# Performance work log

Measured on AMD Instinct MI355X. Metric: run time of the kernel, lower is better.

The kernel has to match this reference:

```python
import jax, jax.numpy as jnp
import numpy as np

IN_SIZE = 784
Z_DIM = 128
K_DIM = 8192
BATCH = 16384
ENC_HIDDEN = [512, 256]          # EncoderMLP default
DEC_SIZES = [Z_DIM, 256, 512, 784]  # DecoderMLP default: [latent, *hidden]


def _linear(x, w, b):
    return x @ w + b


def find_nearest(query, target):
    # Faithful to: sqrt(sum((Q-T)^2, -1)).min(1)[1]; sqrt is monotone so
    # argmin of squared distance is identical. Computed via the GEMM
    # expansion instead of materializing the (N,K,D) broadcast tensor.
    q2 = jnp.sum(query * query, axis=1, keepdims=True)        # [N,1]
    t2 = jnp.sum(target * target, axis=1)                     # [K]
    d2 = q2 - 2.0 * (query @ target.T) + t2[None, :]          # [N,K]
    idx = jnp.argmin(d2, axis=1)
    return target[idx]


def setup_inputs() -> dict:
    key = jax.random.key(0)
    ks = jax.random.split(key, 16)
    s = 0.02
    inp = {"X": jax.random.uniform(ks[0], (BATCH, 1, 28, 28), dtype=jnp.float32)}
    # Encoder: 784 -> 512 -> 256 (mlp blocks, ReLU) -> 128 (plain Linear)
    enc_sizes = [IN_SIZE] + ENC_HIDDEN + [Z_DIM]
    for i, (din, dout) in enumerate(zip(enc_sizes, enc_sizes[1:]), 1):
        inp[f"enc_w{i}"] = s * jax.random.normal(ks[i], (din, dout), dtype=jnp.float32)
        inp[f"enc_b{i}"] = jnp.zeros((dout,), dtype=jnp.float32)
    # Codebook
    inp["codebook"] = jax.random.normal(ks[8], (K_DIM, Z_DIM), dtype=jnp.float32)
    # Decoder: 128 -> 256 -> 512 -> 784 (mlp blocks, ReLU) + sigmoid out
    for i, (din, dout) in enumerate(zip(DEC_SIZES, DEC_SIZES[1:]), 1):
        inp[f"dec_w{i}"] = s * jax.random.normal(ks[8 + i], (din, dout), dtype=jnp.float32)
        inp[f"dec_b{i}"] = jnp.zeros((dout,), dtype=jnp.float32)
    return inp


def reference(X, enc_w1, enc_b1, enc_w2, enc_b2, enc_w3, enc_b3, codebook,
              dec_w1, dec_b1, dec_w2, dec_b2, dec_w3, dec_b3):
    x = X.reshape(-1, IN_SIZE)
    # Encoder (mlp_block = Linear+ReLU, final layer plain Linear)
    h = jax.nn.relu(_linear(x, enc_w1, enc_b1))
    h = jax.nn.relu(_linear(h, enc_w2, enc_b2))
    z_enc = _linear(h, enc_w3, enc_b3)                         # [N, Z]
    # Nearest codebook vector for each encoding
    z_dec = find_nearest(z_enc, codebook)                      # [N, Z]
    # Decoder
    d = jax.nn.relu(_linear(z_dec, dec_w1, dec_b1))
    d = jax.nn.relu(_linear(d, dec_w2, dec_b2))
    d = jax.nn.relu(_linear(d, dec_w3, dec_b3))
    x_recon = jax.nn.sigmoid(d).reshape(-1, 1, 28, 28)
    # Nearest encoding for each codebook vector (for embedding loss)
    z_enc_for_embd = find_nearest(codebook, z_enc)             # [K, Z]
    return (x_recon, z_enc, z_dec, z_enc_for_embd)
```

## Files before the change

### kernel.cpp

```cpp
#include <hip/hip_runtime.h>
#include <math.h>

using u16 = unsigned short;
using u32 = unsigned int;
using u64 = unsigned long long;

typedef __bf16 bf16x8 __attribute__((ext_vector_type(8)));
typedef short  s16x8  __attribute__((ext_vector_type(8)));
typedef float  f32x4  __attribute__((ext_vector_type(4)));

__device__ __forceinline__ float b2f(u16 u){
  union { u32 i; float f; } x; x.i = ((u32)u) << 16; return x.f;
}
__device__ __forceinline__ u16 f2b(float f){
  union { float f; u32 i; } x; x.f = f;
  u32 i = x.i;
  u32 r = (i + 0x7fffu + ((i >> 16) & 1u)) >> 16;
  return (u16)r;
}
__device__ __forceinline__ f32x4 mfma16(s16x8 a, s16x8 b, f32x4 c){
  return __builtin_amdgcn_mfma_f32_16x16x32_bf16(
      __builtin_bit_cast(bf16x8, a), __builtin_bit_cast(bf16x8, b), c, 0, 0, 0);
}
__device__ __forceinline__ u64 shfl_xor_u64(u64 v, int m){
  int lo = __shfl_xor((int)(u32)v, m);
  int hi = __shfl_xor((int)(u32)(v >> 32), m);
  return ((u64)(u32)hi << 32) | (u32)lo;
}
__device__ __forceinline__ u64 umin64(u64 a, u64 b){ return a < b ? a : b; }
__device__ __forceinline__ u64 packmin(float v, int idx){
  u32 b = __float_as_uint(v);
  b = (b & 0x80000000u) ? ~b : (b | 0x80000000u);
  return ((u64)b << 32) | (u32)idx;
}

__global__ __launch_bounds__(256) void canary_k(float* out, float code){
  out[threadIdx.x] = code;
}

__global__ __launch_bounds__(256) void prep_weights(
    const float* __restrict__ w1, const float* __restrict__ w2, const float* __restrict__ w3,
    const float* __restrict__ dw1, const float* __restrict__ dw2, const float* __restrict__ dw3,
    const float* __restrict__ cb,
    u16* __restrict__ o1h, u16* __restrict__ o1l, u16* __restrict__ o2h, u16* __restrict__ o2l,
    u16* __restrict__ o3h, u16* __restrict__ o3l, u16* __restrict__ o4h, u16* __restrict__ o4l,
    u16* __restrict__ o5h, u16* __restrict__ o5l, u16* __restrict__ o6h, u16* __restrict__ o6l,
    u16* __restrict__ cbh, u16* __restrict__ cbl)
{
  size_t o = (size_t)blockIdx.x * 256 + threadIdx.x;
  if (o >= 1155072){
    size_t e = o - 1155072;
    if (e >= 1048576) return;
    float v = cb[e];
    u16 h = f2b(v);
    cbh[e] = h;
    cbl[e] = f2b(v - b2f(h));
    return;
  }
  const float* src; u16 *hi, *lo; int K, N, Kp; size_t base;
  if      (o <  425984){ src=w1;  hi=o1h; lo=o1l; K=784; N=512; Kp=832; base=0; }
  else if (o <  557056){ src=w2;  hi=o2h; lo=o2l; K=512; N=256; Kp=512; base=425984; }
  else if (o <  589824){ src=w3;  hi=o3h; lo=o3l; K=256; N=128; Kp=256; base=557056; }
  else if (o <  622592){ src=dw1; hi=o4h; lo=o4l; K=128; N=256; Kp=128; base=589824; }
  else if (o <  753664){ src=dw2; hi=o5h; lo=o5l; K=256; N=512; Kp=256; base=622592; }
  else                 { src=dw3; hi=o6h; lo=o6l; K=512; N=784; Kp=512; base=753664; }
  size_t e = o - base;
  int n = (int)(e / Kp), kp = (int)(e % Kp);
  u16 h = 0, l = 0;
  if (kp < K){
    float v = src[(size_t)kp * N + n];
    h = f2b(v);
    l = f2b(v - b2f(h));
  }
  hi[e] = h; lo[e] = l;
}

__global__ __launch_bounds__(256) void norms_all(const float* __restrict__ z, const float* __restrict__ cb,
                                                 float* __restrict__ q2, float* __restrict__ t2){
  int i = blockIdx.x * 256 + threadIdx.x;
  const float* src; float* dst;
  if (i < 16384){ src = z + (size_t)i * 128; dst = q2 + i; }
  else { int j = i - 16384; src = cb + (size_t)j * 128; dst = t2 + j; }
  const float4* r = (const float4*)src;
  float s = 0.f;
  for (int k = 0; k < 32; k++){
    float4 p = r[k];
    s += p.x * p.x + p.y * p.y + p.z * p.z + p.w * p.w;
  }
  *dst = s;
}

template<int ACT, int OUTP>
__global__ __launch_bounds__(256, 2) void gemm_af32(
    const float* __restrict__ A, const u16* __restrict__ B0, const u16* __restrict__ B1,
    const float* __restrict__ bias, float* __restrict__ Cf,
    u16* __restrict__ P0, u16* __restrict__ P1,
    int Astr, int KLIM, int Kp, int KT, int N, int nRowsB)
{
  __shared__ __align__(16) u16 Ah[128][72];
  __shared__ __align__(16) u16 Al[128][72];
  __shared__ __align__(16) u16 Bh[128][72];
  __shared__ __align__(16) u16 Bl[128][72];
  const int tid = threadIdx.x;
  const int m0 = blockIdx.y * 128, n0 = blockIdx.x * 128;
  const int wave = tid >> 6, lane = tid & 63;
  const int wm = (wave >> 1) * 64, wn = (wave & 1) * 64;
  const int quad = lane >> 4, l15 = lane & 15;
  f32x4 acc[4][4] = {};

  for (int kt = 0; kt < KT; ++kt){
    const int kb = kt * 64;
    #pragma unroll
    for (int c = 0; c < 8; c++){
      int idx = c * 256 + tid;
      int r = idx >> 4, c4 = (idx & 15) * 4;
      float4 v = make_float4(0.f, 0.f, 0.f, 0.f);
      if (kb + c4 < KLIM)
        v = *(const float4*)(A + (size_t)(m0 + r) * Astr + kb + c4);
      ushort4 h, l;
      h.x = f2b(v.x); l.x = f2b(v.x - b2f(h.x));
      h.y = f2b(v.y); l.y = f2b(v.y - b2f(h.y));
      h.z = f2b(v.z); l.z = f2b(v.z - b2f(h.z));
      h.w = f2b(v.w); l.w = f2b(v.w - b2f(h.w));
      *(ushort4*)&Ah[r][c4] = h;
      *(ushort4*)&Al[r][c4] = l;
    }
    #pragma unroll
    for (int c = 0; c < 4; c++){
      int idx = c * 256 + tid;
      int r = idx >> 3, col = (idx & 7) * 8;
      int rb = n0 + r; rb = rb < nRowsB ? rb : nRowsB - 1;
      *(uint4*)&Bh[r][col] = *(const uint4*)(B0 + (size_t)rb * Kp + kb + col);
      *(uint4*)&Bl[r][col] = *(const uint4*)(B1 + (size_t)rb * Kp + kb + col);
    }
    __syncthreads();
    #pragma unroll
    for (int kh = 0; kh < 2; ++kh){
      s16x8 ah[4], al[4], bh[4], bl[4];
      #pragma unroll
      for (int t4 = 0; t4 < 4; t4++){
        ah[t4] = *(const s16x8*)&Ah[wm + t4 * 16 + l15][kh * 32 + quad * 8];
        al[t4] = *(const s16x8*)&Al[wm + t4 * 16 + l15][kh * 32 + quad * 8];
        bh[t4] = *(const s16x8*)&Bh[wn + t4 * 16 + l15][kh * 32 + quad * 8];
        bl[t4] = *(const s16x8*)&Bl[wn + t4 * 16 + l15][kh * 32 + quad * 8];
      }
      #pragma unroll
      for (int mt = 0; mt < 4; mt++)
        #pragma unroll
        for (int nt = 0; nt < 4; nt++){
          acc[mt][nt] = mfma16(ah[mt], bh[nt], acc[mt][nt]);
          acc[mt][nt] = mfma16(ah[mt], bl[nt], acc[mt][nt]);
          acc[mt][nt] = mfma16(al[mt], bh[nt], acc[mt][nt]);
        }
    }
    __syncthreads();
  }

  float bvs[4]; int cols[4];
  #pragma unroll
  for (int nt = 0; nt < 4; nt++){
    int cN = n0 + wn + nt * 16 + l15;
    cols[nt] = cN;
    int cc = cN < N ? cN : N - 1;
    bvs[nt] = bias[cc];
  }
  #pragma unroll
  for (int mt = 0; mt < 4; mt++){
    int rbase = m0 + wm + mt * 16 + quad * 4;
    #pragma unroll
    for (int nt = 0; nt < 4; nt++){
      if (cols[nt] < N){
        #pragma unroll
        for (int r = 0; r < 4; r++){
          float v = acc[mt][nt][r] + bvs[nt];
          if (ACT >= 1) v = v > 0.f ? v : 0.f;
          if (ACT == 2) v = 1.f / (1.f + expf(-v));
          size_t off = (size_t)(rbase + r) * N + cols[nt];
          if (OUTP == 2){
            P0[off] = f2b(v);
          } else {
            Cf[off] = v;
            if (OUTP == 1){
              u16 h = f2b(v);
              P0[off] = h;
              P1[off] = f2b(v - b2f(h));
            }
          }
        }
      }
    }
  }
}

__global__ __launch_bounds__(256, 1) void dist3(
    const u16* __restrict__ Zh, const u16* __restrict__ Zl,
    const u16* __restrict__ Bh, const u16* __restrict__ Bl,
    const float* __restrict__ q2, const float* __restrict__ t2,
    u64* __restrict__ rowp, u64* __restrict__ colp)
{
  __shared__ u64 sRow[2][128];
  const int tid = threadIdx.x;
  const int i0 = blockIdx.y * 128;
  const int strip = blockIdx.x;
  const int wave = tid >> 6, lane = tid & 63;
  const int wm = (wave >> 1) * 64, wn = (wave & 1) * 64;
  const int quad = lane >> 4, l15 = lane & 15;

  s16x8 zh[2][2][4], zl[2][2][4];
  #pragma unroll
  for (int kb = 0; kb < 2; kb++)
    #pragma unroll
    for (int kh = 0; kh < 2; kh++)
      #pragma unroll
      for (int mt = 0; mt < 4; mt++){
        size_t off = (size_t)(i0 + wm + mt * 16 + l15) * 128 + kb * 64 + kh * 32 + quad * 8;
        zh[kb][kh][mt] = *(const s16x8*)(Zh + off);
        zl[kb][kh][mt] = *(const s16x8*)(Zl + off);
      }
  float qv[4][4];
  #pragma unroll
  for (int mt = 0; mt < 4; mt++)
    #pragma unroll
    for (int r = 0; r < 4; r++)
      qv[mt][r] = q2[i0 + wm + mt * 16 + quad * 4 + r];

  u64 rowm[4][4];
  #pragma unroll
  for (int mt = 0; mt < 4; mt++)
    #pragma unroll
    for (int r = 0; r < 4; r++) rowm[mt][r] = ~0ULL;

  for (int jt = 0; jt < 16; ++jt){
    const int j0 = strip * 2048 + jt * 128;
    f32x4 acc[4][4] = {};
    #pragma unroll
    for (int kb = 0; kb < 2; kb++)
      #pragma unroll
      for (int kh = 0; kh < 2; kh++){
        s16x8 bh[4], bl[4];
        #pragma unroll
        for (int nt = 0; nt < 4; nt++){
          size_t off = (size_t)(j0 + wn + nt * 16 + l15) * 128 + kb * 64 + kh * 32 + quad * 8;
          bh[nt] = *(const s16x8*)(Bh + off);
          bl[nt] = *(const s16x8*)(Bl + off);
        }
        #pragma unroll
        for (int mt = 0; mt < 4; mt++)
          #pragma unroll
          for (int nt = 0; nt < 4; nt++){
            acc[mt][nt] = mfma16(zh[kb][kh][mt], bh[nt], acc[mt][nt]);
            acc[mt][nt] = mfma16(zh[kb][kh][mt], bl[nt], acc[mt][nt]);
            acc[mt][nt] = mfma16(zl[kb][kh][mt], bh[nt], acc[mt][nt]);
            acc[mt][nt] = mfma16(zl[kb][kh][mt], bl[nt], acc[mt][nt]);
          }
      }
    float t2v[4]; int gj[4];
    #pragma unroll
    for (int nt = 0; nt < 4; nt++){
      gj[nt] = j0 + wn + nt * 16 + l15;
      t2v[nt] = t2[gj[nt]];
    }
    #pragma unroll
    for (int mt = 0; mt < 4; mt++){
      #pragma unroll
      for (int r = 0; r < 4; r++){
        float qq = qv[mt][r];
        float rbest = (qq - 2.f * acc[mt][0][r]) + t2v[0];
        int   ridx  = gj[0];
        #pragma unroll
        for (int nt = 1; nt < 4; nt++){
          float v = (qq - 2.f * acc[mt][nt][r]) + t2v[nt];
          if (v < rbest){ rbest = v; ridx = gj[nt]; }
        }
        rowm[mt][r] = umin64(rowm[mt][r], packmin(rbest, ridx));
      }
    }
    #pragma unroll
    for (int nt = 0; nt < 4; nt++){
      float cbest = 3.4e38f; int cidx = 0;
      #pragma unroll
      for (int mt = 0; mt < 4; mt++){
        #pragma unroll
        for (int r = 0; r < 4; r++){
          float vc = (t2v[nt] - 2.f * acc[mt][nt][r]) + qv[mt][r];
          if (vc < cbest){ cbest = vc; cidx = i0 + wm + mt * 16 + quad * 4 + r; }
        }
      }
      u64 p = packmin(cbest, cidx);
      p = umin64(p, shfl_xor_u64(p, 16));
      p = umin64(p, shfl_xor_u64(p, 32));
      if (quad == 0)
        colp[(size_t)(blockIdx.y * 2 + (wave >> 1)) * 8192 + gj[nt]] = p;
    }
  }

  #pragma unroll
  for (int mt = 0; mt < 4; mt++)
    #pragma unroll
    for (int r = 0; r < 4; r++){
      u64 p = rowm[mt][r];
      p = umin64(p, shfl_xor_u64(p, 1));
      p = umin64(p, shfl_xor_u64(p, 2));
      p = umin64(p, shfl_xor_u64(p, 4));
      p = umin64(p, shfl_xor_u64(p, 8));
      rowm[mt][r] = p;
    }
  if (l15 == 0){
    #pragma unroll
    for (int mt = 0; mt < 4; mt++)
      #pragma unroll
      for (int r = 0; r < 4; r++)
        sRow[wave & 1][wm + mt * 16 + quad * 4 + r] = rowm[mt][r];
  }
  __syncthreads();
  if (tid < 128)
    rowp[(size_t)strip * 16384 + i0 + tid] = umin64(sRow[0][tid], sRow[1][tid]);
}

__global__ __launch_bounds__(256) void reduce_rc(
    const u64* __restrict__ rowp, const u64* __restrict__ colp,
    const float* __restrict__ cb, const float* __restrict__ zenc,
    float* __restrict__ zdec, float* __restrict__ zembd, int* __restrict__ rowidx)
{
  int tid = threadIdx.x;
  __shared__ u64 s[4][64];
  __shared__ int sidx[64];
  if (blockIdx.x < 256){
    int base = blockIdx.x * 64;
    int n = base + (tid & 63);
    u64 best = ~0ULL;
    for (int p = tid >> 6; p < 4; p += 4)
      best = umin64(best, rowp[(size_t)p * 16384 + n]);
    s[tid >> 6][tid & 63] = best;
    __syncthreads();
    if (tid < 64){
      u64 b = umin64(umin64(s[0][tid], s[1][tid]), umin64(s[2][tid], s[3][tid]));
      int idx = (int)(b & 0xffffffffULL);
      idx = idx < 0 ? 0 : (idx > 8191 ? 8191 : idx);
      sidx[tid] = idx;
      rowidx[base + tid] = idx;
    }
    __syncthreads();
    for (int q = 0; q < 32; q++){
      int e = q * 256 + tid; int r = e >> 7, c = e & 127;
      zdec[(size_t)(base + r) * 128 + c] = cb[(size_t)sidx[r] * 128 + c];
    }
  } else {
    int base = (blockIdx.x - 256) * 64;
    int n = base + (tid & 63);
    u64 best = ~0ULL;
    for (int p = tid >> 6; p < 256; p += 4)
      best = umin64(best, colp[(size_t)p * 8192 + n]);
    s[tid >> 6][tid & 63] = best;
    __syncthreads();
    if (tid < 64){
      u64 b = umin64(umin64(s[0][tid], s[1][tid]), umin64(s[2][tid], s[3][tid]));
      int idx = (int)(b & 0xffffffffULL);
      idx = idx < 0 ? 0 : (idx > 16383 ? 16383 : idx);
      sidx[tid] = idx;
    }
    __syncthreads();
    for (int q = 0; q < 32; q++){
      int e = q * 256 + tid; int r = e >> 7, c = e & 127;
      zembd[(size_t)(base + r) * 128 + c] = zenc[(size_t)sidx[r] * 128 + c];
    }
  }
}

__global__ __launch_bounds__(256) void gather_xrec(
    const u16* __restrict__ xdecb, const int* __restrict__ rowidx, float* __restrict__ xrec)
{
  size_t o = (size_t)blockIdx.x * 256 + threadIdx.x;
  int row = (int)(o / 784), c = (int)(o % 784);
  int idx = rowidx[row];
  idx = idx < 0 ? 0 : (idx > 8191 ? 8191 : idx);
  xrec[o] = b2f(xdecb[(size_t)idx * 784 + c]);
}

extern "C" void kernel_launch(void* const* d_in, const int* in_sizes, int n_in,
                              void* d_out, int out_size, void* d_ws, size_t ws_size,
                              hipStream_t stream){
  const float* X   = (const float*)d_in[0];
  const float* w1  = (const float*)d_in[1];  const float* b1  = (const float*)d_in[2];
  const float* w2  = (const float*)d_in[3];  const float* b2  = (const float*)d_in[4];
  const float* w3  = (const float*)d_in[5];  const float* b3  = (const float*)d_in[6];
  const float* cb  = (const float*)d_in[7];
  const float* dw1 = (const float*)d_in[8];  const float* db1 = (const float*)d_in[9];
  const float* dw2 = (const float*)d_in[10]; const float* db2 = (const float*)d_in[11];
  const float* dw3 = (const float*)d_in[12]; const float* db3 = (const float*)d_in[13];

  float* out   = (float*)d_out;
  float* xrec  = out;
  float* zenc  = out + 12845056;
  float* zdec  = zenc + 2097152;
  float* zembd = zdec + 2097152;

  const size_t NEEDED = 22085632;
  if (ws_size < NEEDED){
    canary_k<<<1, 256, 0, stream>>>(out, 1000.0f + (float)(ws_size >> 20));
    return;
  }

  char* ob = (char*)d_out;
  float* h1   = (float*)(ob + 0);
  float* g2   = (float*)(ob + 0);
  u16*   zhi  = (u16*)(ob + 33554432);
  u16*   zlo  = (u16*)(ob + 37748736);
  u16*   cbhi = (u16*)(ob + 41943040);
  u16*   cblo = (u16*)(ob + 44040192);

  char* w = (char*)d_ws;
  u16* W1Th = (u16*)(w + 0);        u16* W1Tl = (u16*)(w + 851968);
  u16* W2Th = (u16*)(w + 1703936);  u16* W2Tl = (u16*)(w + 1966080);
  u16* W3Th = (u16*)(w + 2228224);  u16* W3Tl = (u16*)(w + 2293760);
  u16* D1Th = (u16*)(w + 2359296);  u16* D1Tl = (u16*)(w + 2424832);
  u16* D2Th = (u16*)(w + 2490368);  u16* D2Tl = (u16*)(w + 2752512);
  u16* D3Th = (u16*)(w + 3014656);  u16* D3Tl = (u16*)(w + 3817472);
  float* q2f = (float*)(w + 4620288);
  float* t2f = (float*)(w + 4685824);
  int*  rowi = (int*)(w + 4718592);
  u64*  rowp = (u64*)(w + 4784128);
  float* h2   = (float*)(w + 5308416);
  u64*  colp  = (u64*)(w + 5308416);
  float* g1   = (float*)(w + 13697024);
  u16*  xdecb = (u16*)(w + 5308416);

  prep_weights<<<8608, 256, 0, stream>>>(w1, w2, w3, dw1, dw2, dw3, cb,
      W1Th, W1Tl, W2Th, W2Tl, W3Th, W3Tl, D1Th, D1Tl, D2Th, D2Tl, D3Th, D3Tl, cbhi, cblo);

  gemm_af32<1, 0><<<dim3(4, 128), 256, 0, stream>>>(X,  W1Th, W1Tl, b1, h1,   nullptr, nullptr, 784, 784, 832, 13, 512, 512);
  gemm_af32<1, 0><<<dim3(2, 128), 256, 0, stream>>>(h1, W2Th, W2Tl, b2, h2,   nullptr, nullptr, 512, 512, 512,  8, 256, 256);
  gemm_af32<0, 1><<<dim3(1, 128), 256, 0, stream>>>(h2, W3Th, W3Tl, b3, zenc, zhi,     zlo,     256, 256, 256,  4, 128, 128);

  norms_all<<<96, 256, 0, stream>>>(zenc, cb, q2f, t2f);

  dist3<<<dim3(4, 128), 256, 0, stream>>>(zhi, zlo, cbhi, cblo, q2f, t2f, rowp, colp);

  reduce_rc<<<384, 256, 0, stream>>>(rowp, colp, cb, zenc, zdec, zembd, rowi);

  gemm_af32<1, 0><<<dim3(2, 64), 256, 0, stream>>>(cb, D1Th, D1Tl, db1, g1, nullptr, nullptr, 128, 128, 128, 2, 256, 256);
  gemm_af32<1, 0><<<dim3(4, 64), 256, 0, stream>>>(g1, D2Th, D2Tl, db2, g2, nullptr, nullptr, 256, 256, 256, 4, 512, 512);
  gemm_af32<2, 2><<<dim3(7, 64), 256, 0, stream>>>(g2, D3Th, D3Tl, db3, nullptr, xdecb, nullptr, 512, 512, 512, 8, 784, 784);

  gather_xrec<<<50176, 256, 0, stream>>>(xdecb, rowi, xrec);
}
```

Baseline: 594.7 us.

## Stage codebook tiles into swizzled LDS with async global_load_lds double buffering

The distance kernel used to load codebook hi/lo fragments from global memory straight into registers for every tile. It now copies each 128x64 half-K slab into an XOR-swizzled shared-memory buffer with global_load_lds, double-buffered across the two K halves, so the next slab loads while MFMAs run on the current one. Waves then read B fragments from LDS, and s_setprio raises priority around the MFMA blocks. This adds barriers, manual vmcnt waits and 64KB of LDS per block, and the hand-tuned vmcnt counts must match the number of outstanding loads or results will be wrong.

```diff
diff --git a/kernel.cpp b/kernel.cpp
--- a/kernel.cpp
+++ b/kernel.cpp
@@ -32,6 +32,11 @@
   u32 b = __float_as_uint(v);
   b = (b & 0x80000000u) ? ~b : (b | 0x80000000u);
   return ((u64)b << 32) | (u32)idx;
+}
+__device__ __forceinline__ void gload16(const void* g, void* l){
+  __builtin_amdgcn_global_load_lds(
+      (const __attribute__((address_space(1))) unsigned int*)g,
+      (__attribute__((address_space(3))) unsigned int*)l, 16, 0, 0);
 }
 
 __global__ __launch_bounds__(256) void canary_k(float* out, float code){
@@ -198,7 +203,7 @@
     const float* __restrict__ q2, const float* __restrict__ t2,
     u64* __restrict__ rowp, u64* __restrict__ colp)
 {
-  __shared__ u64 sRow[2][128];
+  __shared__ __align__(16) u16 smem[2][16384];
   const int tid = threadIdx.x;
   const int i0 = blockIdx.y * 128;
   const int strip = blockIdx.x;
@@ -206,6 +211,10 @@
   const int wm = (wave >> 1) * 64, wn = (wave & 1) * 64;
   const int quad = lane >> 4, l15 = lane & 15;
 
+  const int swz = (l15 & 7) << 4;
+  const int cof0 = (((quad << 4)     ) ^ swz) >> 1;
+  const int cof1 = (((quad << 4) | 64) ^ swz) >> 1;
+
   s16x8 zh[2][2][4], zl[2][2][4];
   #pragma unroll
   for (int kb = 0; kb < 2; kb++)
@@ -230,36 +239,71 @@
     #pragma unroll
     for (int r = 0; r < 4; r++) rowm[mt][r] = ~0ULL;
 
+  #define STAGE(jt_, kb_, buf_) {                                              \
+    size_t jb = (size_t)(strip * 2048 + (jt_) * 128) * 128 + (kb_) * 64;       \
+    _Pragma("unroll")                                                          \
+    for (int c = 0; c < 4; c++){                                               \
+      int ci = c * 256 + wave * 64 + lane;                                     \
+      int row = ci >> 3;                                                       \
+      size_t g = jb + (size_t)row * 128 + (size_t)(((ci & 7) ^ (row & 7)) * 8);\
+      u16* lp = &smem[buf_][ci * 8];                                           \
+      gload16(Bh + g, lp);                                                     \
+      gload16(Bl + g, lp + 8192);                                              \
+    }                                                                          \
+  }
+
+  #define COMPUTE(buf_, kb_) {                                                 \
+    __builtin_amdgcn_s_setprio(1);                                             \
+    _Pragma("unroll")                                                          \
+    for (int kh = 0; kh < 2; kh++){                                            \
+      const int cof = kh ? cof1 : cof0;                                        \
+      s16x8 bh[4], bl[4];                                                      \
+      _Pragma("unroll")                                                        \
+      for (int nt = 0; nt < 4; nt++){                                          \
+        int off = (wn + nt * 16 + l15) * 64 + cof;                             \
+        bh[nt] = *(const s16x8*)&smem[buf_][off];                              \
+        bl[nt] = *(const s16x8*)&smem[buf_][8192 + off];                       \
+      }                                                                        \
+      _Pragma("unroll")                                                        \
+      for (int mt = 0; mt < 4; mt++)                                           \
+        _Pragma("unroll")                                                      \
+        for (int nt = 0; nt < 4; nt++){                                        \
+          acc[mt][nt] = mfma16(zh[kb_][kh][mt], bh[nt], acc[mt][nt]);          \
+          acc[mt][nt] = mfma16(zh[kb_][kh][mt], bl[nt], acc[mt][nt]);          \
+          acc[mt][nt] = mfma16(zl[kb_][kh][mt], bh[nt], acc[mt][nt]);          \
+          acc[mt][nt] = mfma16(zl[kb_][kh][mt], bl[nt], acc[mt][nt]);          \
+        }                                                                      \
+    }                                                                          \
+    __builtin_amdgcn_s_setprio(0);                                             \
+  }
+
+  STAGE(0, 0, 0);
+
+  #pragma unroll 1
   for (int jt = 0; jt < 16; ++jt){
     const int j0 = strip * 2048 + jt * 128;
-    f32x4 acc[4][4] = {};
-    #pragma unroll
-    for (int kb = 0; kb < 2; kb++)
-      #pragma unroll
-      for (int kh = 0; kh < 2; kh++){
-        s16x8 bh[4], bl[4];
-        #pragma unroll
-        for (int nt = 0; nt < 4; nt++){
-          size_t off = (size_t)(j0 + wn + nt * 16 + l15) * 128 + kb * 64 + kh * 32 + quad * 8;
-          bh[nt] = *(const s16x8*)(Bh + off);
-          bl[nt] = *(const s16x8*)(Bl + off);
-        }
-        #pragma unroll
-        for (int mt = 0; mt < 4; mt++)
-          #pragma unroll
-          for (int nt = 0; nt < 4; nt++){
-            acc[mt][nt] = mfma16(zh[kb][kh][mt], bh[nt], acc[mt][nt]);
-            acc[mt][nt] = mfma16(zh[kb][kh][mt], bl[nt], acc[mt][nt]);
-            acc[mt][nt] = mfma16(zl[kb][kh][mt], bh[nt], acc[mt][nt]);
-            acc[mt][nt] = mfma16(zl[kb][kh][mt], bl[nt], acc[mt][nt]);
-          }
-      }
     float t2v[4]; int gj[4];
     #pragma unroll
     for (int nt = 0; nt < 4; nt++){
       gj[nt] = j0 + wn + nt * 16 + l15;
       t2v[nt] = t2[gj[nt]];
     }
+    f32x4 acc[4][4] = {};
+
+    STAGE(jt, 1, 1);
+    asm volatile("s_waitcnt vmcnt(8)" ::: "memory");
+    __builtin_amdgcn_s_barrier();
+    COMPUTE(0, 0)
+    __builtin_amdgcn_s_barrier();
+    if (jt < 15){
+      STAGE(jt + 1, 0, 0);
+      asm volatile("s_waitcnt vmcnt(8)" ::: "memory");
+    } else {
+      asm volatile("s_waitcnt vmcnt(0)" ::: "memory");
+    }
+    __builtin_amdgcn_s_barrier();
+    COMPUTE(1, 1)
+
     #pragma unroll
     for (int mt = 0; mt < 4; mt++){
       #pragma unroll
@@ -292,7 +336,10 @@
       if (quad == 0)
         colp[(size_t)(blockIdx.y * 2 + (wave >> 1)) * 8192 + gj[nt]] = p;
     }
-  }
+    __builtin_amdgcn_s_barrier();
+  }
+  #undef STAGE
+  #undef COMPUTE
 
   #pragma unroll
   for (int mt = 0; mt < 4; mt++)
@@ -305,16 +352,17 @@
       p = umin64(p, shfl_xor_u64(p, 8));
       rowm[mt][r] = p;
     }
+  u64* sRow = (u64*)&smem[0][0];
   if (l15 == 0){
     #pragma unroll
     for (int mt = 0; mt < 4; mt++)
       #pragma unroll
       for (int r = 0; r < 4; r++)
-        sRow[wave & 1][wm + mt * 16 + quad * 4 + r] = rowm[mt][r];
+        sRow[(wave & 1) * 128 + wm + mt * 16 + quad * 4 + r] = rowm[mt][r];
   }
   __syncthreads();
   if (tid < 128)
-    rowp[(size_t)strip * 16384 + i0 + tid] = umin64(sRow[0][tid], sRow[1][tid]);
+    rowp[(size_t)strip * 16384 + i0 + tid] = umin64(sRow[tid], sRow[128 + tid]);
 }
 
 __global__ __launch_bounds__(256) void reduce_rc(
```

Result: no change. 587.0 us (-1.3%).
